# Performance work log

Measured on AMD Instinct MI355X. Metric: run time of the kernel, lower is better.

Reference implementation:

```python
import jax, jax.numpy as jnp
import numpy as np

H = 4          # num_heads
DK = 128       # head_k_dim = hidden*expand_k/H = 1024*0.5/4
DV = 256       # head_v_dim = hidden*expand_v/H
LOW_RANK = 16  # gate_low_rank_dim
GATE_NORM = 16.0  # gate_logit_normalizer
CHUNK = 64
EPS = 1e-5


def setup_inputs() -> dict:
    key = jax.random.key(0)
    ks = jax.random.split(key, 10)
    Dm = 1024
    Kd, Vd = H * DK, H * DV  # key_dim=512, value_dim=1024
    def lin(k, fan_in, fan_out):
        return jax.random.normal(k, (fan_in, fan_out), jnp.float32) * (fan_in ** -0.5)
    return {
        "x": jax.random.normal(ks[0], (4, 2048, Dm), jnp.float32),
        "Wq": lin(ks[1], Dm, Kd),
        "Wk": lin(ks[2], Dm, Kd),
        "Wv": lin(ks[3], Dm, Vd),
        "Wg": lin(ks[4], Dm, Vd),            # output gate proj
        "Wgk1": lin(ks[5], Dm, LOW_RANK),     # low-rank gate proj (no bias)
        "Wgk2": lin(ks[6], LOW_RANK, Kd),     # second gate proj (with bias)
        "bgk2": jnp.zeros((Kd,), jnp.float32),
        "Wo": lin(ks[7], Vd, Dm),
        "gnw": jnp.ones((DV,), jnp.float32),  # FusedRMSNormGated weight
    }


def _gla_chunk(q, k, v, gk):
    """Exact chunkwise evaluation of the GLA recurrence:
       S_t = diag(exp(gk_t)) S_{t-1} + k_t^T v_t;  o_t = scale * q_t S_t.
       q,k,gk: [B,T,H,DK], v: [B,T,H,DV]."""
    B, T, _, _ = q.shape
    NC, C = T // CHUNK, CHUNK
    scale = DK ** -0.5
    def chunks(a):  # [B,T,H,D] -> [NC,B,H,C,D]
        return a.reshape(B, NC, C, H, a.shape[-1]).transpose(1, 0, 3, 2, 4)
    qc, kc, vc, gc = chunks(q), chunks(k), chunks(v), chunks(gk)
    G = jnp.cumsum(gc, axis=-2)                    # within-chunk cumulative log-decay
    qg = qc * jnp.exp(G) * scale                   # q_i exp(G_i)
    k_intra = kc * jnp.exp(-G)                     # k_j exp(-G_j)
    kg = kc * jnp.exp(G[..., -1:, :] - G)          # k_j exp(G_C - G_j) for state update
    g_last = jnp.exp(G[..., -1, :])                # exp(G_C): per-chunk total decay
    # intra-chunk causal attention (diagonal included)
    A = jnp.einsum('nbhik,nbhjk->nbhij', qg, k_intra)
    A = jnp.where(jnp.tril(jnp.ones((C, C), bool)), A, 0.0)
    o_intra = jnp.einsum('nbhij,nbhjv->nbhiv', A, vc)
    def step(S, inp):
        qg_, kg_, v_, gl_, oi_ = inp
        o = oi_ + jnp.einsum('bhck,bhkv->bhcv', qg_, S)
        S = S * gl_[..., :, None] + jnp.einsum('bhck,bhcv->bhkv', kg_, v_)
        return S, o
    S0 = jnp.zeros((B, H, DK, DV), q.dtype)
    _, o = jax.lax.scan(step, S0, (qg, kg, vc, g_last, o_intra))
    return o.transpose(1, 0, 3, 2, 4).reshape(B, T, H, DV)


def reference(x, Wq, Wk, Wv, Wg, Wgk1, Wgk2, bgk2, Wo, gnw):
    B, T, Dm = x.shape
    q = (x @ Wq).reshape(B, T, H, DK)
    k = (x @ Wk).reshape(B, T, H, DK)
    v = (x @ Wv).reshape(B, T, H, DV)
    gk = jax.nn.log_sigmoid((x @ Wgk1) @ Wgk2 + bgk2) / GATE_NORM
    gk = gk.reshape(B, T, H, DK)
    o = _gla_chunk(q, k, v, gk)                              # [B,T,H,DV]
    g = (x @ Wg).reshape(B, T, H, DV)
    # FusedRMSNormGated: RMSNorm(o) * weight * swish(g)
    o = o * jax.lax.rsqrt(jnp.mean(o * o, axis=-1, keepdims=True) + EPS) * gnw
    o = o * (g * jax.nn.sigmoid(g))
    return o.reshape(B, T, H * DV) @ Wo
```

## Files before the change

### kernel.cpp

```cpp
#include <hip/hip_runtime.h>
#include <hip/hip_bf16.h>
#include <stdint.h>

#define B_  4
#define T_  2048
#define DM  1024
#define H_  4
#define DK_ 128
#define DV_ 256
#define KD  512
#define VD  1024
#define NCH 32
#define CC  64
#define BT  8192
#define SCALE 0.08838834764831845f
#define GNORM_INV 0.0625f

typedef __attribute__((ext_vector_type(8))) short short8;
typedef __attribute__((ext_vector_type(4))) float f32x4;
typedef uint32_t u32;
typedef unsigned short ushort_t;

__device__ inline ushort_t f2b(float f) {
    u32 u = __builtin_bit_cast(u32, f);
    u32 r = (u + 0x7fffu + ((u >> 16) & 1u)) >> 16;
    return (ushort_t)r;
}
__device__ inline void unpack2(u32 u, float& lo, float& hi) {
    lo = __builtin_bit_cast(float, u << 16);
    hi = __builtin_bit_cast(float, u & 0xffff0000u);
}
__device__ inline void gload_lds16(const void* g, void* l) {
    __builtin_amdgcn_global_load_lds(
        (const __attribute__((address_space(1))) uint32_t*)g,
        (__attribute__((address_space(3))) uint32_t*)l, 16, 0, 0);
}

__global__ __launch_bounds__(256)
void cvtx(const float* __restrict__ x, ushort_t* __restrict__ xb, int n) {
    int idx = (blockIdx.x * 256 + threadIdx.x) * 8;
    if (idx >= n) return;
    float4 a = *(const float4*)&x[idx];
    float4 b = *(const float4*)&x[idx + 4];
    uint4 p;
    p.x = (u32)f2b(a.x) | ((u32)f2b(a.y) << 16);
    p.y = (u32)f2b(a.z) | ((u32)f2b(a.w) << 16);
    p.z = (u32)f2b(b.x) | ((u32)f2b(b.y) << 16);
    p.w = (u32)f2b(b.z) | ((u32)f2b(b.w) << 16);
    *(uint4*)&xb[idx] = p;
}

__global__ __launch_bounds__(256)
void tcvt(const float* __restrict__ W, ushort_t* __restrict__ Wt, int K, int N) {
    __shared__ float tile[32][33];
    const int k0 = blockIdx.x * 32, n0 = blockIdx.y * 32;
    const int r = threadIdx.x >> 3, c4 = (threadIdx.x & 7) * 4;
    float4 wv = *(const float4*)&W[(size_t)(k0 + r) * N + n0 + c4];
    tile[r][c4 + 0] = wv.x; tile[r][c4 + 1] = wv.y;
    tile[r][c4 + 2] = wv.z; tile[r][c4 + 3] = wv.w;
    __syncthreads();
    u32 lo = (u32)f2b(tile[c4 + 0][r]) | ((u32)f2b(tile[c4 + 1][r]) << 16);
    u32 hi = (u32)f2b(tile[c4 + 2][r]) | ((u32)f2b(tile[c4 + 3][r]) << 16);
    uint2 o2; o2.x = lo; o2.y = hi;
    *(uint2*)&Wt[(size_t)(n0 + r) * K + k0 + c4] = o2;
}

template<int OUTBF>
__global__ __launch_bounds__(256)
void gemm_bf16(const ushort_t* __restrict__ A, const ushort_t* __restrict__ Bt,
               void* __restrict__ Cout, int M, int N, int K) {
    __shared__ ushort_t Al[128 * 32];
    __shared__ ushort_t Bl[128 * 32];
    const int t = threadIdx.x;
    const int wave = t >> 6, lane = t & 63;
    const int wr = wave >> 1, wc = wave & 1;
    const int row0 = blockIdx.x * 128, col0 = blockIdx.y * 128;
    const int lm = lane & 15, lk = (lane >> 4) * 8;

    const int b0 = t * 16;
    const int r0 = b0 >> 6, c0 = (b0 & 63) >> 1;
    const int r1 = (4096 + b0) >> 6, c1 = ((4096 + b0) & 63) >> 1;
    ushort_t* ldsA0 = &Al[(wave * 1024) >> 1];
    ushort_t* ldsA1 = &Al[(4096 + wave * 1024) >> 1];
    ushort_t* ldsB0 = &Bl[(wave * 1024) >> 1];
    ushort_t* ldsB1 = &Bl[(4096 + wave * 1024) >> 1];

    f32x4 acc[4][4];
    #pragma unroll
    for (int i = 0; i < 4; ++i)
        #pragma unroll
        for (int j = 0; j < 4; ++j) acc[i][j] = f32x4{0.f, 0.f, 0.f, 0.f};

    const ushort_t* Ap = A + (size_t)row0 * K;
    const ushort_t* Bp = Bt + (size_t)col0 * K;

    for (int k0 = 0; k0 < K; k0 += 32) {
        __syncthreads();
        gload_lds16(Ap + (size_t)r0 * K + k0 + c0, ldsA0);
        gload_lds16(Ap + (size_t)r1 * K + k0 + c1, ldsA1);
        gload_lds16(Bp + (size_t)r0 * K + k0 + c0, ldsB0);
        gload_lds16(Bp + (size_t)r1 * K + k0 + c1, ldsB1);
        __syncthreads();
        short8 af[4], bfr[4];
        #pragma unroll
        for (int f = 0; f < 4; ++f)
            af[f] = *(const short8*)(&Al[(wr * 64 + f * 16 + lm) * 32 + lk]);
        #pragma unroll
        for (int f = 0; f < 4; ++f)
            bfr[f] = *(const short8*)(&Bl[(wc * 64 + f * 16 + lm) * 32 + lk]);
        #pragma unroll
        for (int i = 0; i < 4; ++i)
            #pragma unroll
            for (int j = 0; j < 4; ++j)
                acc[i][j] = __builtin_amdgcn_mfma_f32_16x16x32_bf16(af[i], bfr[j], acc[i][j], 0, 0, 0);
    }
    const int orow = row0 + wr * 64 + (lane >> 4) * 4;
    const int ocol = col0 + wc * 64 + lm;
    #pragma unroll
    for (int i = 0; i < 4; ++i)
        #pragma unroll
        for (int j = 0; j < 4; ++j)
            #pragma unroll
            for (int e = 0; e < 4; ++e) {
                int rr = orow + i * 16 + e, cc = ocol + j * 16;
                if (OUTBF) ((ushort_t*)Cout)[(size_t)rr * N + cc] = f2b(acc[i][j][e]);
                else       ((float*)Cout)[(size_t)rr * N + cc]   = acc[i][j][e];
            }
}

__global__ __launch_bounds__(256)
void lowrank_kernel(const float* __restrict__ x, const float* __restrict__ W1,
                    float* __restrict__ tmp) {
    __shared__ float part[16][20];
    const int row = blockIdx.x;
    const int t = threadIdx.x;
    const int ks = t >> 4, c = t & 15;
    const float* xp = x + (size_t)row * DM + ks * 64;
    const float* wp0 = W1 + (size_t)(ks * 64) * 16 + c;
    float acc = 0.f;
    #pragma unroll
    for (int i = 0; i < 16; ++i) {
        float4 xv = *(const float4*)&xp[i * 4];
        const float* wp = wp0 + i * 64;
        acc += xv.x * wp[0] + xv.y * wp[16] + xv.z * wp[32] + xv.w * wp[48];
    }
    part[ks][c] = acc;
    __syncthreads();
    if (t < 16) {
        float s = 0.f;
        #pragma unroll
        for (int i = 0; i < 16; ++i) s += part[i][t];
        tmp[row * 16 + t] = s;
    }
}

__global__ __launch_bounds__(256)
void gatek_kernel(const float* __restrict__ tmp, const float* __restrict__ W2,
                  const float* __restrict__ bias, float* __restrict__ gk) {
    const int idx = blockIdx.x * 256 + threadIdx.x;
    const int bt = idx >> 9, c = idx & 511;
    float z = bias[c];
    #pragma unroll
    for (int j = 0; j < 16; ++j)
        z += tmp[bt * 16 + j] * W2[j * KD + c];
    float ls = fminf(z, 0.f) - log1pf(expf(-fabsf(z)));
    gk[idx] = ls * GNORM_INV;
}

__global__ __launch_bounds__(128)
void gateprep_kernel(const float* __restrict__ q, const float* __restrict__ kf,
                     const float* __restrict__ gk,
                     ushort_t* __restrict__ qgb, ushort_t* __restrict__ kib,
                     ushort_t* __restrict__ kgb, float* __restrict__ glast) {
    const int bid = blockIdx.x;
    const int c = bid & 31, bh = bid >> 5;
    const int b = bh >> 2, h = bh & 3;
    const int d = threadIdx.x;
    const int t0 = b * T_ + c * CC;
    const int gbase = t0 * KD + h * DK_ + d;
    const int obase = bid * (CC * DK_) + d;

    float total = 0.f;
    for (int i = 0; i < CC; ++i) total += gk[gbase + i * KD];

    float G = 0.f;
    for (int i = 0; i < CC; ++i) {
        const int gi = gbase + i * KD;
        G += gk[gi];
        float qv = q[gi], kv = kf[gi];
        qgb[obase + i * DK_] = f2b(qv * expf(G) * SCALE);
        kib[obase + i * DK_] = f2b(kv * expf(-G));
        kgb[obase + i * DK_] = f2b(kv * expf(total - G));
    }
    glast[bid * DK_ + d] = expf(total);
}

__global__ __launch_bounds__(256)
void vtrans_kernel(const ushort_t* __restrict__ vbf, ushort_t* __restrict__ vT) {
    __shared__ ushort_t vl[64][264];
    const int bid = blockIdx.x;
    const int c = bid & 31, bh = bid >> 5;
    const int b = bh >> 2, h = bh & 3;
    const int t0 = b * T_ + c * CC;
    const int t = threadIdx.x;

    #pragma unroll
    for (int m = 0; m < 8; ++m) {
        int p = t + m * 256;
        int j = p >> 5, d8 = (p & 31) * 8;
        *(uint4*)&vl[j][d8] = *(const uint4*)&vbf[(size_t)(t0 + j) * VD + h * DV_ + d8];
    }
    __syncthreads();

    const size_t outb = (size_t)bid * (256 * 64);
    #pragma unroll
    for (int it = 0; it < 2; ++it) {
        int dv = it * 128 + (t >> 1);
        int j0 = (t & 1) * 32;
        u32 vv[16];
        #pragma unroll
        for (int wi = 0; wi < 16; ++wi)
            vv[wi] = (u32)vl[j0 + 2 * wi][dv] | ((u32)vl[j0 + 2 * wi + 1][dv] << 16);
        ushort_t* dst = &vT[outb + (size_t)dv * 64 + j0];
        *(uint4*)(dst + 0)  = make_uint4(vv[0], vv[1], vv[2], vv[3]);
        *(uint4*)(dst + 8)  = make_uint4(vv[4], vv[5], vv[6], vv[7]);
        *(uint4*)(dst + 16) = make_uint4(vv[8], vv[9], vv[10], vv[11]);
        *(uint4*)(dst + 24) = make_uint4(vv[12], vv[13], vv[14], vv[15]);
    }
}

__global__ __launch_bounds__(256)
void chunk_state(const ushort_t* __restrict__ kgb, const ushort_t* __restrict__ vT,
                 ushort_t* __restrict__ Sst) {
    __shared__ ushort_t kgT[128 * 72];
    const int bid = blockIdx.x;
    const int t = threadIdx.x;
    const size_t kgbase = (size_t)bid * (CC * DK_);
    const size_t vtbase = (size_t)bid * (256 * 64);
    const size_t sbase  = (size_t)bid * (256 * 128);

    #pragma unroll
    for (int m = 0; m < 4; ++m) {
        int p = t + m * 256;
        int j = p >> 4, d0 = (p & 15) * 8;
        uint4 r = *(const uint4*)&kgb[kgbase + (size_t)j * DK_ + d0];
        kgT[(d0 + 0) * 72 + j] = (ushort_t)(r.x & 0xffff);
        kgT[(d0 + 1) * 72 + j] = (ushort_t)(r.x >> 16);
        kgT[(d0 + 2) * 72 + j] = (ushort_t)(r.y & 0xffff);
        kgT[(d0 + 3) * 72 + j] = (ushort_t)(r.y >> 16);
        kgT[(d0 + 4) * 72 + j] = (ushort_t)(r.z & 0xffff);
        kgT[(d0 + 5) * 72 + j] = (ushort_t)(r.z >> 16);
        kgT[(d0 + 6) * 72 + j] = (ushort_t)(r.w & 0xffff);
        kgT[(d0 + 7) * 72 + j] = (ushort_t)(r.w >> 16);
    }
    __syncthreads();

    const int w = t >> 6, lane = t & 63;
    const int lm = lane & 15, lg = lane >> 4;
    #pragma unroll
    for (int mm = 0; mm < 4; ++mm) {
        const int mt = w * 4 + mm;
        short8 a0 = *(const short8*)&vT[vtbase + (size_t)(mt * 16 + lm) * 64 + lg * 8];
        short8 a1 = *(const short8*)&vT[vtbase + (size_t)(mt * 16 + lm) * 64 + 32 + lg * 8];
        #pragma unroll
        for (int n = 0; n < 8; ++n) {
            f32x4 acc = {0.f, 0.f, 0.f, 0.f};
            short8 b0 = *(const short8*)&kgT[(n * 16 + lm) * 72 + lg * 8];
            short8 b1 = *(const short8*)&kgT[(n * 16 + lm) * 72 + 32 + lg * 8];
            acc = __builtin_amdgcn_mfma_f32_16x16x32_bf16(a0, b0, acc, 0, 0, 0);
            acc = __builtin_amdgcn_mfma_f32_16x16x32_bf16(a1, b1, acc, 0, 0, 0);
            #pragma unroll
            for (int e = 0; e < 4; ++e)
                Sst[sbase + (size_t)(mt * 16 + lg * 4 + e) * 128 + n * 16 + lm] = f2b(acc[e]);
        }
    }
}

__global__ __launch_bounds__(256)
void scan_combine(ushort_t* __restrict__ Sst, const float* __restrict__ glast) {
    const int bid = blockIdx.x;
    const int dvt = bid & 15, bh = bid >> 4;
    const int t = threadIdx.x;
    const int dv = dvt * 16 + (t >> 4);
    const int dk0 = (t & 15) * 8;

    float P[8];
    #pragma unroll
    for (int e = 0; e < 8; ++e) P[e] = 0.f;

    for (int c = 0; c < NCH; ++c) {
        const size_t base = ((size_t)(bh * NCH + c) * 256 + dv) * 128 + dk0;
        uint4 m0 = *(const uint4*)&Sst[base];
        u32 wd[4];
        #pragma unroll
        for (int e = 0; e < 4; ++e)
            wd[e] = (u32)f2b(P[2 * e]) | ((u32)f2b(P[2 * e + 1]) << 16);
        *(uint4*)&Sst[base] = make_uint4(wd[0], wd[1], wd[2], wd[3]);
        float mv[8];
        unpack2(m0.x, mv[0], mv[1]); unpack2(m0.y, mv[2], mv[3]);
        unpack2(m0.z, mv[4], mv[5]); unpack2(m0.w, mv[6], mv[7]);
        const float* glp = &glast[(size_t)(bh * NCH + c) * DK_ + dk0];
        float4 g0 = *(const float4*)&glp[0];
        float4 g1 = *(const float4*)&glp[4];
        float gl[8] = {g0.x, g0.y, g0.z, g0.w, g1.x, g1.y, g1.z, g1.w};
        #pragma unroll
        for (int e = 0; e < 8; ++e) P[e] = gl[e] * P[e] + mv[e];
    }
}

__global__ __launch_bounds__(256)
void fused_chunk(const ushort_t* __restrict__ qgb, const ushort_t* __restrict__ kib,
                 const ushort_t* __restrict__ vT, const ushort_t* __restrict__ Sst,
                 ushort_t* __restrict__ ob) {
    __shared__ __align__(16) ushort_t lds[24064];
    ushort_t* stg = lds;
    ushort_t* vq  = lds + 10752;
    ushort_t* Al  = lds + 17408;

    const int bid = blockIdx.x;
    const int c = bid & 31, bh = bid >> 5;
    const int b = bh >> 2, h = bh & 3;
    const int t0 = b * T_ + c * CC;
    const int t = threadIdx.x;
    const int w = t >> 6, lane = t & 63;
    const int lm = lane & 15, lg = lane >> 4;
    const int m0 = w * 16;

    const size_t qbase  = (size_t)bid * (CC * DK_);
    const size_t vtbase = (size_t)bid * (256 * 64);
    const size_t sbase  = (size_t)bid * (256 * 128);

    short8 qf[4];
    #pragma unroll
    for (int kk = 0; kk < 4; ++kk)
        qf[kk] = *(const short8*)&qgb[qbase + (size_t)(m0 + lm) * DK_ + kk * 32 + lg * 8];

    #pragma unroll
    for (int m = 0; m < 4; ++m) {
        int p = t + m * 256;
        int j = p >> 4, d0 = (p & 15) * 8;
        *(uint4*)&stg[j * 168 + d0] = *(const uint4*)&kib[qbase + (size_t)j * DK_ + d0];
    }
    __syncthreads();

    f32x4 accA[4];
    #pragma unroll
    for (int jt = 0; jt < 4; ++jt) accA[jt] = f32x4{0.f, 0.f, 0.f, 0.f};
    #pragma unroll
    for (int jt = 0; jt < 4; ++jt)
        #pragma unroll
        for (int kk = 0; kk < 4; ++kk) {
            short8 bfrag = *(const short8*)&stg[(jt * 16 + lm) * 168 + kk * 32 + lg * 8];
            accA[jt] = __builtin_amdgcn_mfma_f32_16x16x32_bf16(qf[kk], bfrag, accA[jt], 0, 0, 0);
        }
    #pragma unroll
    for (int jt = 0; jt < 4; ++jt)
        #pragma unroll
        for (int e = 0; e < 4; ++e) {
            int i = m0 + lg * 4 + e, j = jt * 16 + lm;
            Al[i * 104 + j] = f2b(j <= i ? accA[jt][e] : 0.f);
        }
    __syncthreads();

    short8 af[2];
    #pragma unroll
    for (int kk = 0; kk < 2; ++kk)
        af[kk] = *(const short8*)&Al[(m0 + lm) * 104 + kk * 32 + lg * 8];

    #pragma unroll 1
    for (int qq = 0; qq < 4; ++qq) {
        #pragma unroll
        for (int m = 0; m < 2; ++m) {
            int p = t + m * 256;
            int dvr = p >> 3, d0 = (p & 7) * 8;
            *(uint4*)&vq[dvr * 104 + d0] =
                *(const uint4*)&vT[vtbase + (size_t)(qq * 64 + dvr) * 64 + d0];
        }
        #pragma unroll
        for (int m = 0; m < 4; ++m) {
            int p = t + m * 256;
            int dvr = p >> 4, d0 = (p & 15) * 8;
            *(uint4*)&stg[dvr * 168 + d0] =
                *(const uint4*)&Sst[sbase + (size_t)(qq * 64 + dvr) * 128 + d0];
        }
        __syncthreads();
        #pragma unroll
        for (int n = 0; n < 4; ++n) {
            f32x4 acc = {0.f, 0.f, 0.f, 0.f};
            #pragma unroll
            for (int kk = 0; kk < 2; ++kk) {
                short8 bfrag = *(const short8*)&vq[(n * 16 + lm) * 104 + kk * 32 + lg * 8];
                acc = __builtin_amdgcn_mfma_f32_16x16x32_bf16(af[kk], bfrag, acc, 0, 0, 0);
            }
            #pragma unroll
            for (int kk = 0; kk < 4; ++kk) {
                short8 bfrag = *(const short8*)&stg[(n * 16 + lm) * 168 + kk * 32 + lg * 8];
                acc = __builtin_amdgcn_mfma_f32_16x16x32_bf16(qf[kk], bfrag, acc, 0, 0, 0);
            }
            #pragma unroll
            for (int e = 0; e < 4; ++e)
                ob[(size_t)(t0 + m0 + lg * 4 + e) * VD + h * DV_ + qq * 64 + n * 16 + lm] = f2b(acc[e]);
        }
        __syncthreads();
    }
}

__global__ __launch_bounds__(256)
void normgate_kernel(const ushort_t* __restrict__ ob, const ushort_t* __restrict__ gbf,
                     const float* __restrict__ gnw, ushort_t* __restrict__ obf) {
    const int t = threadIdx.x;
    const int w = t >> 6, lane = t & 63;
    const int row = blockIdx.x * 4 + w;
    const size_t base = (size_t)row * DV_ + lane * 4;

    uint2 ov2 = *(const uint2*)&ob[base];
    float o0v, o1v, o2v, o3v;
    unpack2(ov2.x, o0v, o1v); unpack2(ov2.y, o2v, o3v);
    float ssq = o0v * o0v + o1v * o1v + o2v * o2v + o3v * o3v;
    #pragma unroll
    for (int off = 32; off > 0; off >>= 1) ssq += __shfl_xor(ssq, off);
    const float rms = rsqrtf(ssq * (1.0f / DV_) + 1e-5f);

    uint2 gv2 = *(const uint2*)&gbf[base];
    float g0, g1, g2, g3;
    unpack2(gv2.x, g0, g1); unpack2(gv2.y, g2, g3);
    float4 wv = *(const float4*)&gnw[lane * 4];
    float r0 = o0v * rms * wv.x * (g0 / (1.f + expf(-g0)));
    float r1 = o1v * rms * wv.y * (g1 / (1.f + expf(-g1)));
    float r2 = o2v * rms * wv.z * (g2 / (1.f + expf(-g2)));
    float r3 = o3v * rms * wv.w * (g3 / (1.f + expf(-g3)));
    uint2 p;
    p.x = (u32)f2b(r0) | ((u32)f2b(r1) << 16);
    p.y = (u32)f2b(r2) | ((u32)f2b(r3) << 16);
    *(uint2*)&obf[base] = p;
}

extern "C" void kernel_launch(void* const* d_in, const int* in_sizes, int n_in,
                              void* d_out, int out_size, void* d_ws, size_t ws_size,
                              hipStream_t stream) {
    const float* x    = (const float*)d_in[0];
    const float* Wq   = (const float*)d_in[1];
    const float* Wk   = (const float*)d_in[2];
    const float* Wv   = (const float*)d_in[3];
    const float* Wg   = (const float*)d_in[4];
    const float* Wgk1 = (const float*)d_in[5];
    const float* Wgk2 = (const float*)d_in[6];
    const float* bgk2 = (const float*)d_in[7];
    const float* Wo   = (const float*)d_in[8];
    const float* gnw  = (const float*)d_in[9];

    float* ws = (float*)d_ws;
    float* q      = ws;
    float* kf     = ws + 4194304;
    float* gk     = ws + 8388608;
    ushort_t* vT  = (ushort_t*)(ws + 12582912);
    ushort_t* Sst = (ushort_t*)(ws + 16777216);
    ushort_t* vbf = (ushort_t*)(ws + 16777216);
    ushort_t* wbf = (ushort_t*)(ws + 20971520);
    ushort_t* gbf = (ushort_t*)(ws + 8388608);
    ushort_t* obf = (ushort_t*)(ws + 16777216);
    ushort_t* ob  = (ushort_t*)ws;
    ushort_t* xbf = (ushort_t*)(ws + 25165824);
    ushort_t* qgb = (ushort_t*)(ws + 29360128);
    ushort_t* kib = (ushort_t*)(ws + 31457280);
    ushort_t* kgb = (ushort_t*)(ws + 33554432);
    float* tmp16  = ws + 35651584;
    float* glast  = ws + 35782656;

    cvtx<<<4096, 256, 0, stream>>>(x, xbf, BT * DM);

    tcvt<<<dim3(32, 16), 256, 0, stream>>>(Wq, wbf, DM, KD);
    gemm_bf16<0><<<dim3(64, 4), 256, 0, stream>>>(xbf, wbf, q, BT, KD, DM);
    tcvt<<<dim3(32, 16), 256, 0, stream>>>(Wk, wbf, DM, KD);
    gemm_bf16<0><<<dim3(64, 4), 256, 0, stream>>>(xbf, wbf, kf, BT, KD, DM);
    tcvt<<<dim3(32, 32), 256, 0, stream>>>(Wv, wbf, DM, VD);
    gemm_bf16<1><<<dim3(64, 8), 256, 0, stream>>>(xbf, wbf, vbf, BT, VD, DM);

    lowrank_kernel<<<8192, 256, 0, stream>>>(x, Wgk1, tmp16);
    gatek_kernel<<<16384, 256, 0, stream>>>(tmp16, Wgk2, bgk2, gk);
    gateprep_kernel<<<512, 128, 0, stream>>>(q, kf, gk, qgb, kib, kgb, glast);

    vtrans_kernel<<<512, 256, 0, stream>>>(vbf, vT);

    tcvt<<<dim3(32, 32), 256, 0, stream>>>(Wg, wbf, DM, VD);
    gemm_bf16<1><<<dim3(64, 8), 256, 0, stream>>>(xbf, wbf, gbf, BT, VD, DM);

    chunk_state<<<512, 256, 0, stream>>>(kgb, vT, Sst);
    scan_combine<<<256, 256, 0, stream>>>(Sst, glast);
    fused_chunk<<<512, 256, 0, stream>>>(qgb, kib, vT, Sst, ob);

    normgate_kernel<<<8192, 256, 0, stream>>>(ob, gbf, gnw, obf);
    tcvt<<<dim3(32, 32), 256, 0, stream>>>(Wo, wbf, VD, DM);
    gemm_bf16<0><<<dim3(64, 8), 256, 0, stream>>>(obf, wbf, (float*)d_out, BT, DM, VD);
}
```

Measured before the change: 402.6 us.

## Fuse Q/K/V projections into one GEMM, use MFMA for low-rank gate, swizzle tiles

Concatenates the transposed Wq, Wk and Wv into one bf16 weight and runs a single GEMM that writes q/k as fp32 and v as bf16, so the x tile is read once and two launches go away. The low-rank gate projection now reads the bf16 x through MFMA instead of doing scalar fp32 dot products. GEMM launches use a 1D grid with a block-index swizzle meant to improve L2 reuse. The gateprep loops gain unroll pragmas. The low-rank projection now runs in bf16, which slightly lowers gate precision.

```diff
diff --git a/kernel.cpp b/kernel.cpp
--- a/kernel.cpp
+++ b/kernel.cpp
@@ -65,16 +65,104 @@
     *(uint2*)&Wt[(size_t)(n0 + r) * K + k0 + c4] = o2;
 }
 
-template<int OUTBF>
-__global__ __launch_bounds__(256)
-void gemm_bf16(const ushort_t* __restrict__ A, const ushort_t* __restrict__ Bt,
-               void* __restrict__ Cout, int M, int N, int K) {
+__global__ __launch_bounds__(256)
+void w1trans(const float* __restrict__ W1, ushort_t* __restrict__ w1t) {
+    int idx = blockIdx.x * 256 + threadIdx.x;
+    int k = idx >> 4, n = idx & 15;
+    w1t[n * 1024 + k] = f2b(W1[k * 16 + n]);
+}
+
+__global__ __launch_bounds__(256)
+void gemm_qkv(const ushort_t* __restrict__ A, const ushort_t* __restrict__ Bt,
+              float* __restrict__ qo, float* __restrict__ ko,
+              ushort_t* __restrict__ vo) {
     __shared__ ushort_t Al[128 * 32];
     __shared__ ushort_t Bl[128 * 32];
+    const int wg = blockIdx.x;
+    const int swz = (wg & 7) * 128 + (wg >> 3);
+    const int bx = swz & 63, by = swz >> 6;
     const int t = threadIdx.x;
     const int wave = t >> 6, lane = t & 63;
     const int wr = wave >> 1, wc = wave & 1;
-    const int row0 = blockIdx.x * 128, col0 = blockIdx.y * 128;
+    const int row0 = bx * 128, col0 = by * 128;
+    const int lm = lane & 15, lk = (lane >> 4) * 8;
+
+    const int b0 = t * 16;
+    const int r0 = b0 >> 6, c0 = (b0 & 63) >> 1;
+    const int r1 = (4096 + b0) >> 6, c1 = ((4096 + b0) & 63) >> 1;
+    ushort_t* ldsA0 = &Al[(wave * 1024) >> 1];
+    ushort_t* ldsA1 = &Al[(4096 + wave * 1024) >> 1];
+    ushort_t* ldsB0 = &Bl[(wave * 1024) >> 1];
+    ushort_t* ldsB1 = &Bl[(4096 + wave * 1024) >> 1];
+
+    f32x4 acc[4][4];
+    #pragma unroll
+    for (int i = 0; i < 4; ++i)
+        #pragma unroll
+        for (int j = 0; j < 4; ++j) acc[i][j] = f32x4{0.f, 0.f, 0.f, 0.f};
+
+    const ushort_t* Ap = A + (size_t)row0 * DM;
+    const ushort_t* Bp = Bt + (size_t)col0 * DM;
+
+    for (int k0 = 0; k0 < DM; k0 += 32) {
+        __syncthreads();
+        gload_lds16(Ap + (size_t)r0 * DM + k0 + c0, ldsA0);
+        gload_lds16(Ap + (size_t)r1 * DM + k0 + c1, ldsA1);
+        gload_lds16(Bp + (size_t)r0 * DM + k0 + c0, ldsB0);
+        gload_lds16(Bp + (size_t)r1 * DM + k0 + c1, ldsB1);
+        __syncthreads();
+        short8 af[4], bfr[4];
+        #pragma unroll
+        for (int f = 0; f < 4; ++f)
+            af[f] = *(const short8*)(&Al[(wr * 64 + f * 16 + lm) * 32 + lk]);
+        #pragma unroll
+        for (int f = 0; f < 4; ++f)
+            bfr[f] = *(const short8*)(&Bl[(wc * 64 + f * 16 + lm) * 32 + lk]);
+        #pragma unroll
+        for (int i = 0; i < 4; ++i)
+            #pragma unroll
+            for (int j = 0; j < 4; ++j)
+                acc[i][j] = __builtin_amdgcn_mfma_f32_16x16x32_bf16(af[i], bfr[j], acc[i][j], 0, 0, 0);
+    }
+    const int orow = row0 + wr * 64 + (lane >> 4) * 4;
+    const int cbase = col0 + wc * 64 + lm;
+    if (by < 8) {
+        float* C = (by < 4) ? qo : ko;
+        const int cc0 = cbase - ((by < 4) ? 0 : 512);
+        #pragma unroll
+        for (int i = 0; i < 4; ++i)
+            #pragma unroll
+            for (int j = 0; j < 4; ++j)
+                #pragma unroll
+                for (int e = 0; e < 4; ++e)
+                    C[(size_t)(orow + i * 16 + e) * KD + cc0 + j * 16] = acc[i][j][e];
+    } else {
+        const int cc0 = cbase - 1024;
+        #pragma unroll
+        for (int i = 0; i < 4; ++i)
+            #pragma unroll
+            for (int j = 0; j < 4; ++j)
+                #pragma unroll
+                for (int e = 0; e < 4; ++e)
+                    vo[(size_t)(orow + i * 16 + e) * VD + cc0 + j * 16] = f2b(acc[i][j][e]);
+    }
+}
+
+template<int OUTBF>
+__global__ __launch_bounds__(256)
+void gemm_bf16(const ushort_t* __restrict__ A, const ushort_t* __restrict__ Bt,
+               void* __restrict__ Cout, int M, int N, int K, int nbx) {
+    __shared__ ushort_t Al[128 * 32];
+    __shared__ ushort_t Bl[128 * 32];
+    const int nwg = gridDim.x;
+    const int cpx = nwg >> 3;
+    const int wg = blockIdx.x;
+    const int swz = (wg & 7) * cpx + (wg >> 3);
+    const int bx = swz % nbx, by = swz / nbx;
+    const int t = threadIdx.x;
+    const int wave = t >> 6, lane = t & 63;
+    const int wr = wave >> 1, wc = wave & 1;
+    const int row0 = bx * 128, col0 = by * 128;
     const int lm = lane & 15, lk = (lane >> 4) * 8;
 
     const int b0 = t * 16;
@@ -129,29 +217,22 @@
 }
 
 __global__ __launch_bounds__(256)
-void lowrank_kernel(const float* __restrict__ x, const float* __restrict__ W1,
-                    float* __restrict__ tmp) {
-    __shared__ float part[16][20];
-    const int row = blockIdx.x;
-    const int t = threadIdx.x;
-    const int ks = t >> 4, c = t & 15;
-    const float* xp = x + (size_t)row * DM + ks * 64;
-    const float* wp0 = W1 + (size_t)(ks * 64) * 16 + c;
-    float acc = 0.f;
-    #pragma unroll
-    for (int i = 0; i < 16; ++i) {
-        float4 xv = *(const float4*)&xp[i * 4];
-        const float* wp = wp0 + i * 64;
-        acc += xv.x * wp[0] + xv.y * wp[16] + xv.z * wp[32] + xv.w * wp[48];
-    }
-    part[ks][c] = acc;
-    __syncthreads();
-    if (t < 16) {
-        float s = 0.f;
-        #pragma unroll
-        for (int i = 0; i < 16; ++i) s += part[i][t];
-        tmp[row * 16 + t] = s;
-    }
+void lowrank_mfma(const ushort_t* __restrict__ xbf, const ushort_t* __restrict__ w1t,
+                  float* __restrict__ tmp) {
+    const int t = threadIdx.x;
+    const int w = t >> 6, lane = t & 63;
+    const int lm = lane & 15, lg = lane >> 4;
+    const int row0 = blockIdx.x * 64 + w * 16;
+    f32x4 acc = {0.f, 0.f, 0.f, 0.f};
+    #pragma unroll
+    for (int kk = 0; kk < 32; ++kk) {
+        short8 a = *(const short8*)&xbf[(size_t)(row0 + lm) * DM + kk * 32 + lg * 8];
+        short8 b = *(const short8*)&w1t[(size_t)lm * DM + kk * 32 + lg * 8];
+        acc = __builtin_amdgcn_mfma_f32_16x16x32_bf16(a, b, acc, 0, 0, 0);
+    }
+    #pragma unroll
+    for (int e = 0; e < 4; ++e)
+        tmp[(size_t)(row0 + lg * 4 + e) * 16 + lm] = acc[e];
 }
 
 __global__ __launch_bounds__(256)
@@ -181,9 +262,11 @@
     const int obase = bid * (CC * DK_) + d;
 
     float total = 0.f;
+    #pragma unroll 8
     for (int i = 0; i < CC; ++i) total += gk[gbase + i * KD];
 
     float G = 0.f;
+    #pragma unroll 4
     for (int i = 0; i < CC; ++i) {
         const int gi = gbase + i * KD;
         G += gk[gi];
@@ -450,46 +533,48 @@
     const float* gnw  = (const float*)d_in[9];
 
     float* ws = (float*)d_ws;
-    float* q      = ws;
-    float* kf     = ws + 4194304;
-    float* gk     = ws + 8388608;
-    ushort_t* vT  = (ushort_t*)(ws + 12582912);
-    ushort_t* Sst = (ushort_t*)(ws + 16777216);
-    ushort_t* vbf = (ushort_t*)(ws + 16777216);
-    ushort_t* wbf = (ushort_t*)(ws + 20971520);
-    ushort_t* gbf = (ushort_t*)(ws + 8388608);
-    ushort_t* obf = (ushort_t*)(ws + 16777216);
-    ushort_t* ob  = (ushort_t*)ws;
-    ushort_t* xbf = (ushort_t*)(ws + 25165824);
-    ushort_t* qgb = (ushort_t*)(ws + 29360128);
-    ushort_t* kib = (ushort_t*)(ws + 31457280);
-    ushort_t* kgb = (ushort_t*)(ws + 33554432);
-    float* tmp16  = ws + 35651584;
-    float* glast  = ws + 35782656;
+    float* q       = ws;
+    float* kf      = ws + 4194304;
+    float* gk      = ws + 8388608;
+    ushort_t* vT   = (ushort_t*)(ws + 12582912);
+    ushort_t* Sst  = (ushort_t*)(ws + 16777216);
+    ushort_t* vbf  = (ushort_t*)(ws + 16777216);
+    ushort_t* wcat = (ushort_t*)(ws + 20971520);
+    ushort_t* wgt  = (ushort_t*)(ws + 22020096);
+    ushort_t* obf  = (ushort_t*)(ws + 16777216);
+    ushort_t* wbfO = (ushort_t*)(ws + 20971520);
+    ushort_t* ob   = (ushort_t*)ws;
+    ushort_t* gbf  = (ushort_t*)(ws + 4194304);
+    ushort_t* xbf  = (ushort_t*)(ws + 25165824);
+    ushort_t* qgb  = (ushort_t*)(ws + 29360128);
+    ushort_t* kib  = (ushort_t*)(ws + 31457280);
+    ushort_t* kgb  = (ushort_t*)(ws + 33554432);
+    float* tmp16   = ws + 35651584;
+    float* glast   = ws + 35782656;
+    ushort_t* w1t  = (ushort_t*)(ws + 35848192);
 
     cvtx<<<4096, 256, 0, stream>>>(x, xbf, BT * DM);
-
-    tcvt<<<dim3(32, 16), 256, 0, stream>>>(Wq, wbf, DM, KD);
-    gemm_bf16<0><<<dim3(64, 4), 256, 0, stream>>>(xbf, wbf, q, BT, KD, DM);
-    tcvt<<<dim3(32, 16), 256, 0, stream>>>(Wk, wbf, DM, KD);
-    gemm_bf16<0><<<dim3(64, 4), 256, 0, stream>>>(xbf, wbf, kf, BT, KD, DM);
-    tcvt<<<dim3(32, 32), 256, 0, stream>>>(Wv, wbf, DM, VD);
-    gemm_bf16<1><<<dim3(64, 8), 256, 0, stream>>>(xbf, wbf, vbf, BT, VD, DM);
-
-    lowrank_kernel<<<8192, 256, 0, stream>>>(x, Wgk1, tmp16);
+    w1trans<<<64, 256, 0, stream>>>(Wgk1, w1t);
+
+    tcvt<<<dim3(32, 16), 256, 0, stream>>>(Wq, wcat, DM, KD);
+    tcvt<<<dim3(32, 16), 256, 0, stream>>>(Wk, wcat + (size_t)512 * 1024, DM, KD);
+    tcvt<<<dim3(32, 32), 256, 0, stream>>>(Wv, wcat + (size_t)1024 * 1024, DM, VD);
+    tcvt<<<dim3(32, 32), 256, 0, stream>>>(Wg, wgt, DM, VD);
+
+    gemm_qkv<<<1024, 256, 0, stream>>>(xbf, wcat, q, kf, vbf);
+
+    lowrank_mfma<<<128, 256, 0, stream>>>(xbf, w1t, tmp16);
     gatek_kernel<<<16384, 256, 0, stream>>>(tmp16, Wgk2, bgk2, gk);
     gateprep_kernel<<<512, 128, 0, stream>>>(q, kf, gk, qgb, kib, kgb, glast);
 
+    gemm_bf16<1><<<512, 256, 0, stream>>>(xbf, wgt, gbf, BT, VD, DM, 64);
+
     vtrans_kernel<<<512, 256, 0, stream>>>(vbf, vT);
-
-    tcvt<<<dim3(32, 32), 256, 0, stream>>>(Wg, wbf, DM, VD);
-    gemm_bf16<1><<<dim3(64, 8), 256, 0, stream>>>(xbf, wbf, gbf, BT, VD, DM);
-
     chunk_state<<<512, 256, 0, stream>>>(kgb, vT, Sst);
     scan_combine<<<256, 256, 0, stream>>>(Sst, glast);
     fused_chunk<<<512, 256, 0, stream>>>(qgb, kib, vT, Sst, ob);
 
+    tcvt<<<dim3(32, 32), 256, 0, stream>>>(Wo, wbfO, VD, DM);
     normgate_kernel<<<8192, 256, 0, stream>>>(ob, gbf, gnw, obf);
-    tcvt<<<dim3(32, 32), 256, 0, stream>>>(Wo, wbf, VD, DM);
-    gemm_bf16<0><<<dim3(64, 8), 256, 0, stream>>>(obf, wbf, (float*)d_out, BT, DM, VD);
-}
+    gemm_bf16<0><<<512, 256, 0, stream>>>(obf, wbfO, (float*)d_out, BT, DM, VD, 64);
+}
```

New measurement: 360.1 us. 10.6% less time.
